# Optimization experiments

Hardware: AMD Instinct MI355X
Metric: run time of the kernel (lower is better)

## Reference

```python
import jax, jax.numpy as jnp
import numpy as np

N, IN, OUT, H = 8192, 128, 64, 4
NEG_SLOPE = 0.2   # GATConv leaky-relu slope
EPS = 1e-5        # BatchNorm1d eps
MASK_VAL = -1e9   # masked_fill value for non-edges (finite for grad safety)


def setup_inputs() -> dict:
    key = jax.random.key(0)
    ks = jax.random.split(key, 5)
    x = jax.random.normal(ks[0], (N, IN), jnp.float32)
    adj = jax.random.randint(ks[1], (N, N), 0, 2, jnp.int32)  # dense 0/1 adjacency
    W = jax.random.normal(ks[2], (H, IN, OUT), jnp.float32) * (1.0 / np.sqrt(IN))
    a_i = jax.random.normal(ks[3], (H, OUT), jnp.float32) * (1.0 / np.sqrt(OUT))
    a_j = jax.random.normal(ks[4], (H, OUT), jnp.float32) * (1.0 / np.sqrt(OUT))
    gamma = jnp.ones((H * OUT,), jnp.float32)   # BN weight
    beta = jnp.zeros((H * OUT,), jnp.float32)   # BN bias
    return {"x": x, "adj": adj, "W": W, "a_i": a_i, "a_j": a_j,
            "gamma": gamma, "beta": beta}


def reference(x, adj, W, a_i, a_j, gamma, beta):
    # --- GATConv (dense adjacency, multi-head, concat) ---
    h = jnp.einsum('ni,hio->hno', x, W)              # [H, N, OUT]
    ei = jnp.einsum('hno,ho->hn', h, a_i)            # [H, N] source scores
    ej = jnp.einsum('hno,ho->hn', h, a_j)            # [H, N] target scores
    coe = ei[:, :, None] + ej[:, None, :]            # [H, N, N]
    coe = jnp.where(coe >= 0, coe, NEG_SLOPE * coe)  # leaky_relu
    coe = jnp.where(adj[None, :, :] == 0, MASK_VAL, coe)
    att = jax.nn.softmax(coe, axis=-1)               # segment softmax over neighbors
    out = jnp.einsum('hnm,hmo->hno', att, h)         # weighted aggregation
    out = jnp.transpose(out, (1, 0, 2)).reshape(N, H * OUT)  # concat heads
    # --- BatchNorm1d (training-mode batch stats over nodes) ---
    mean = jnp.mean(out, axis=0)
    var = jnp.var(out, axis=0)
    out = (out - mean) * jax.lax.rsqrt(var + EPS) * gamma + beta
    # --- ReLU ---
    return jax.nn.relu(out)
```

## Files before the change

### kernel.cpp

```cpp
#include <hip/hip_runtime.h>
#include <hip/hip_bf16.h>

#define NN   8192
#define IND  128
#define OUTD 64
#define NH   4
#define NEG_SLOPE 0.2f
#define BN_EPS 1e-5f

typedef __attribute__((ext_vector_type(8))) short bf16x8;
typedef __attribute__((ext_vector_type(4))) float f32x4;
typedef __attribute__((ext_vector_type(4))) int   i32x4;

static __device__ __forceinline__ short f2bf(float f) {
    union { float f; unsigned u; } v; v.f = f;
    return (short)((v.u + 0x8000u) >> 16);
}

__global__ __launch_bounds__(256) void k0_repackW(const float* __restrict__ W,
                                                  short* __restrict__ WB) {
    int tid = blockIdx.x * 256 + threadIdx.x;
    int o = tid & 63, i = (tid >> 6) & 127, h = tid >> 13;
    WB[((h * 16 + (i >> 3)) * 64 + o) * 8 + (i & 7)] = f2bf(W[(h * 128 + i) * 64 + o]);
}

__global__ __launch_bounds__(256) void k1_feat(const float* __restrict__ x,
                                               const short* __restrict__ WB,
                                               const float* __restrict__ a_i,
                                               const float* __restrict__ a_j,
                                               short* __restrict__ hB,
                                               float* __restrict__ t_Ri,
                                               float* __restrict__ t_E1j, float* __restrict__ t_E2j) {
    int w = threadIdx.x >> 6;
    int l = threadIdx.x & 63;
    int quad = l >> 4, lx = l & 15;
    int rb = blockIdx.x;

    f32x4 acc[4] = {};
#pragma unroll
    for (int ks = 0; ks < 4; ++ks) {
        const float* xp = x + (rb * 16 + lx) * IND + ks * 32 + quad * 8;
        f32x4 xa = *(const f32x4*)xp;
        f32x4 xb = *(const f32x4*)(xp + 4);
        bf16x8 af;
#pragma unroll
        for (int j = 0; j < 4; ++j) { af[j] = f2bf(xa[j]); af[4 + j] = f2bf(xb[j]); }
#pragma unroll
        for (int ot = 0; ot < 4; ++ot) {
            bf16x8 bf = *(const bf16x8*)(WB + ((w * 16 + ks * 4 + quad) * 64 + ot * 16 + lx) * 8);
            acc[ot] = __builtin_amdgcn_mfma_f32_16x16x32_bf16(af, bf, acc[ot], 0, 0, 0);
        }
    }
    float aiv[4], ajv[4];
#pragma unroll
    for (int ot = 0; ot < 4; ++ot) {
        aiv[ot] = a_i[w * 64 + ot * 16 + lx];
        ajv[ot] = a_j[w * 64 + ot * 16 + lx];
    }
#pragma unroll
    for (int reg = 0; reg < 4; ++reg) {
        int row = rb * 16 + quad * 4 + reg;
        float ei = 0.f, ej = 0.f;
#pragma unroll
        for (int ot = 0; ot < 4; ++ot) {
            float hv = acc[ot][reg];
            ei += hv * aiv[ot];
            ej += hv * ajv[ot];
        }
#pragma unroll
        for (int m = 1; m <= 8; m <<= 1) {
            ei += __shfl_xor(ei, m, 64);
            ej += __shfl_xor(ej, m, 64);
        }
        if (lx == reg) {
            t_Ri [w * NN + row] = expf(-0.8f * ei);
            t_E1j[w * NN + row] = expf(ej);
            t_E2j[w * NN + row] = expf(NEG_SLOPE * ej);
        }
#pragma unroll
        for (int ot = 0; ot < 4; ++ot) {
            int o = ot * 16 + lx;
            hB[((w * 1024 + (row >> 3)) * 64 + o) * 8 + (row & 7)] = f2bf(acc[ot][reg]);
        }
    }
}

__global__ __launch_bounds__(256) void k2_attn(const int* __restrict__ adj,
                                               const short* __restrict__ hB,
                                               const float* __restrict__ t_Ri,
                                               const float* __restrict__ t_E1j,
                                               const float* __restrict__ t_E2j,
                                               float* __restrict__ num,
                                               float* __restrict__ Lsum) {
    __shared__ unsigned char smask[64 * 260];
    int tid = threadIdx.x;
    int w = tid >> 6;
    int l = tid & 63;
    int quad = l >> 4, lx = l & 15;
    int rb = blockIdx.x >> 2, ks = blockIdx.x & 3;
    int rowbase = rb * 64;
    int tb = w * NN;
    int k0 = ks * 2048;

    {
        int kc = tid * 8;
#pragma unroll 2
        for (int i = 0; i < 64; ++i) {
            const int* ap = adj + (size_t)(rowbase + i) * NN + k0 + kc;
            i32x4 a0 = *(const i32x4*)ap;
            i32x4 a1 = *(const i32x4*)(ap + 4);
            unsigned m = 0;
#pragma unroll
            for (int j = 0; j < 4; ++j) {
                m |= (a0[j] ? 1u : 0u) << j;
                m |= (a1[j] ? 1u : 0u) << (4 + j);
            }
            smask[i * 260 + tid] = (unsigned char)m;
        }
    }
    __syncthreads();

    float Riv[4];
    int mrow[4];
#pragma unroll
    for (int r = 0; r < 4; ++r) {
        int i = rowbase + r * 16 + lx;
        Riv[r] = t_Ri[tb + i];
        mrow[r] = (r * 16 + lx) * 260 + quad;
    }

    bf16x8 onesf;
#pragma unroll
    for (int j = 0; j < 8; ++j) onesf[j] = (short)0x3F80;

    f32x4 acc[4][4] = {};
    f32x4 accL[4] = {};
    f32x4 pe10, pe11, pe20, pe21;
    bf16x8 pbf[4];
    {
        int kb = k0 + quad * 8;
        pe10 = *(const f32x4*)(t_E1j + tb + kb);
        pe11 = *(const f32x4*)(t_E1j + tb + kb + 4);
        pe20 = *(const f32x4*)(t_E2j + tb + kb);
        pe21 = *(const f32x4*)(t_E2j + tb + kb + 4);
#pragma unroll
        for (int ot = 0; ot < 4; ++ot)
            pbf[ot] = *(const bf16x8*)(hB + ((w * 1024 + (kb >> 3)) * 64 + ot * 16 + lx) * 8);
    }

#pragma unroll 1
    for (int kt = 0; kt < 64; ++kt) {
        f32x4 e1j0 = pe10, e1j1 = pe11;
        f32x4 e2j0 = pe20, e2j1 = pe21;
        bf16x8 bfrag[4];
#pragma unroll
        for (int ot = 0; ot < 4; ++ot) bfrag[ot] = pbf[ot];

        int ktn = (kt + 1) & 63;
        int kbn = k0 + ktn * 32 + quad * 8;
        pe10 = *(const f32x4*)(t_E1j + tb + kbn);
        pe11 = *(const f32x4*)(t_E1j + tb + kbn + 4);
        pe20 = *(const f32x4*)(t_E2j + tb + kbn);
        pe21 = *(const f32x4*)(t_E2j + tb + kbn + 4);
#pragma unroll
        for (int ot = 0; ot < 4; ++ot)
            pbf[ot] = *(const bf16x8*)(hB + ((w * 1024 + (kbn >> 3)) * 64 + ot * 16 + lx) * 8);

        int mc[4];
#pragma unroll
        for (int r = 0; r < 4; ++r) mc[r] = smask[mrow[r] + kt * 4];

        bf16x8 afr[4];
#pragma unroll
        for (int r = 0; r < 4; ++r) {
            union { i32x4 i; bf16x8 b; } af;
#pragma unroll
            for (int jj = 0; jj < 4; ++jj) {
                int j0 = 2 * jj, j1 = 2 * jj + 1;
                float e1A = (j0 < 4) ? e1j0[j0] : e1j1[j0 - 4];
                float e1B = (j1 < 4) ? e1j0[j1] : e1j1[j1 - 4];
                float e2A = (j0 < 4) ? e2j0[j0] : e2j1[j0 - 4];
                float e2B = (j1 < 4) ? e2j0[j1] : e2j1[j1 - 4];
                float p0 = fmaxf(e1A, Riv[r] * e2A);
                float p1 = fmaxf(e1B, Riv[r] * e2B);
                p0 = (mc[r] & (1 << j0)) ? p0 : 0.0f;
                p1 = (mc[r] & (1 << j1)) ? p1 : 0.0f;
                af.i[jj] = (int)__builtin_amdgcn_perm(__float_as_uint(p1),
                                                      __float_as_uint(p0),
                                                      0x07060302);
            }
            afr[r] = af.b;
        }
#pragma unroll
        for (int r = 0; r < 4; ++r)
            accL[r] = __builtin_amdgcn_mfma_f32_16x16x32_bf16(afr[r], onesf, accL[r], 0, 0, 0);
#pragma unroll
        for (int r = 0; r < 4; ++r)
#pragma unroll
            for (int ot = 0; ot < 4; ++ot)
                acc[r][ot] = __builtin_amdgcn_mfma_f32_16x16x32_bf16(afr[r], bfrag[ot], acc[r][ot], 0, 0, 0);
    }

#pragma unroll
    for (int r = 0; r < 4; ++r)
        if (lx == 0)
#pragma unroll
            for (int reg = 0; reg < 4; ++reg)
                atomicAdd(&Lsum[w * NN + rowbase + r * 16 + quad * 4 + reg], accL[r][reg]);
#pragma unroll
    for (int r = 0; r < 4; ++r)
#pragma unroll
        for (int ot = 0; ot < 4; ++ot)
#pragma unroll
            for (int reg = 0; reg < 4; ++reg) {
                int row = rowbase + r * 16 + quad * 4 + reg;
                atomicAdd(&num[row * 256 + w * 64 + ot * 16 + lx], acc[r][ot][reg]);
            }
}

__global__ __launch_bounds__(256) void k3_stats(const float* __restrict__ num,
                                                const float* __restrict__ Lsum,
                                                float* __restrict__ stats) {
    int c = threadIdx.x;
    int h = c >> 6;
    float s = 0.f, s2 = 0.f;
#pragma unroll
    for (int rr = 0; rr < 8; ++rr) {
        int row = blockIdx.x * 8 + rr;
        float val = num[row * 256 + c] / Lsum[h * NN + row];
        s += val; s2 += val * val;
    }
    atomicAdd(&stats[c], s);
    atomicAdd(&stats[c + 256], s2);
}

__global__ __launch_bounds__(256) void k5_apply(const float* __restrict__ num,
                                                const float* __restrict__ Lsum,
                                                const float* __restrict__ stats,
                                                const float* __restrict__ gamma,
                                                const float* __restrict__ beta,
                                                float* __restrict__ out) {
    __shared__ float sbnp[512];
    int c = threadIdx.x;
    float mean = stats[c] * (1.0f / NN);
    float var  = stats[c + 256] * (1.0f / NN) - mean * mean;
    float sc = gamma[c] * rsqrtf(var + BN_EPS);
    sbnp[c] = sc;
    sbnp[c + 256] = beta[c] - mean * sc;
    __syncthreads();

    int g = blockIdx.x * 256 + threadIdx.x;
    f32x4 v = *(const f32x4*)(num + (size_t)g * 4);
    int cb = (g * 4) & 255;
    int row = g >> 6;
    float rL = 1.0f / Lsum[(cb >> 6) * NN + row];
    f32x4 r;
#pragma unroll
    for (int j = 0; j < 4; ++j)
        r[j] = fmaxf((v[j] * rL) * sbnp[cb + j] + sbnp[256 + cb + j], 0.0f);
    *(f32x4*)(out + (size_t)g * 4) = r;
}

extern "C" void kernel_launch(void* const* d_in, const int* in_sizes, int n_in,
                              void* d_out, int out_size, void* d_ws, size_t ws_size,
                              hipStream_t stream) {
    (void)in_sizes; (void)n_in; (void)out_size; (void)ws_size;
    const float* x     = (const float*)d_in[0];
    const int*   adj   = (const int*)d_in[1];
    const float* W     = (const float*)d_in[2];
    const float* a_i   = (const float*)d_in[3];
    const float* a_j   = (const float*)d_in[4];
    const float* gamma = (const float*)d_in[5];
    const float* beta  = (const float*)d_in[6];
    float* out = (float*)d_out;

    char* ws = (char*)d_ws;
    short* WB    = (short*)(ws + 0);
    short* hB    = (short*)(ws + 65536);
    float* t_Ri  = (float*)(ws + 4259840);
    float* t_E1j = t_Ri + 32768;
    float* t_E2j = t_Ri + 2 * 32768;
    float* num   = (float*)(ws + 4784128);
    float* Lsum  = (float*)(ws + 13172736);
    float* stats = (float*)(ws + 13303808);

    hipMemsetAsync(num, 0, 8388608 + 131072 + 2048, stream);

    k0_repackW<<<dim3(128),  dim3(256), 0, stream>>>(W, WB);
    k1_feat   <<<dim3(512),  dim3(256), 0, stream>>>(x, WB, a_i, a_j, hB,
                                                     t_Ri, t_E1j, t_E2j);
    k2_attn   <<<dim3(512),  dim3(256), 0, stream>>>(adj, hB, t_Ri, t_E1j, t_E2j,
                                                     num, Lsum);
    k3_stats  <<<dim3(1024), dim3(256), 0, stream>>>(num, Lsum, stats);
    k5_apply  <<<dim3(2048), dim3(256), 0, stream>>>(num, Lsum, stats, gamma, beta, out);
}
```

Before: 481.6 us.

## Split attention K range into eight chunks and pack mask into per-lane words

The attention kernel now splits the neighbor dimension into eight chunks of 1024 instead of four of 2048, which doubles the grid to 1024 blocks for better occupancy and load balance across CUs. The shared-memory mask is rearranged so each lane reads one 32-bit word holding the mask bytes for its four row groups. That word is prefetched one iteration ahead, replacing four byte loads per step. The cost is twice as many partial-sum atomics or writes into num and Lsum, plus more per-block setup.

```diff
diff --git a/kernel.cpp b/kernel.cpp
--- a/kernel.cpp
+++ b/kernel.cpp
@@ -92,21 +92,25 @@
                                                const float* __restrict__ t_E2j,
                                                float* __restrict__ num,
                                                float* __restrict__ Lsum) {
-    __shared__ unsigned char smask[64 * 260];
+    __shared__ unsigned int swords[128 * 17];
     int tid = threadIdx.x;
     int w = tid >> 6;
     int l = tid & 63;
     int quad = l >> 4, lx = l & 15;
-    int rb = blockIdx.x >> 2, ks = blockIdx.x & 3;
+    int rb = blockIdx.x >> 3, ks = blockIdx.x & 7;
     int rowbase = rb * 64;
     int tb = w * NN;
-    int k0 = ks * 2048;
+    int k0 = ks * 1024;
 
     {
-        int kc = tid * 8;
-#pragma unroll 2
-        for (int i = 0; i < 64; ++i) {
-            const int* ap = adj + (size_t)(rowbase + i) * NN + k0 + kc;
+        unsigned char* sbytes = (unsigned char*)swords;
+        int c = tid & 127;
+        int rhalf = tid >> 7;
+        const int* ap0 = adj + (size_t)(rowbase + rhalf) * NN + k0 + c * 8;
+#pragma unroll 4
+        for (int pass = 0; pass < 32; ++pass) {
+            int row = pass * 2 + rhalf;
+            const int* ap = ap0 + (size_t)(pass * 2) * NN;
             i32x4 a0 = *(const i32x4*)ap;
             i32x4 a1 = *(const i32x4*)(ap + 4);
             unsigned m = 0;
@@ -115,19 +119,15 @@
                 m |= (a0[j] ? 1u : 0u) << j;
                 m |= (a1[j] ? 1u : 0u) << (4 + j);
             }
-            smask[i * 260 + tid] = (unsigned char)m;
+            sbytes[(c * 17 + (row & 15)) * 4 + (row >> 4)] = (unsigned char)m;
         }
     }
     __syncthreads();
 
     float Riv[4];
-    int mrow[4];
-#pragma unroll
-    for (int r = 0; r < 4; ++r) {
-        int i = rowbase + r * 16 + lx;
-        Riv[r] = t_Ri[tb + i];
-        mrow[r] = (r * 16 + lx) * 260 + quad;
-    }
+#pragma unroll
+    for (int r = 0; r < 4; ++r)
+        Riv[r] = t_Ri[tb + rowbase + r * 16 + lx];
 
     bf16x8 onesf;
 #pragma unroll
@@ -137,6 +137,7 @@
     f32x4 accL[4] = {};
     f32x4 pe10, pe11, pe20, pe21;
     bf16x8 pbf[4];
+    unsigned pmw;
     {
         int kb = k0 + quad * 8;
         pe10 = *(const f32x4*)(t_E1j + tb + kb);
@@ -146,17 +147,19 @@
 #pragma unroll
         for (int ot = 0; ot < 4; ++ot)
             pbf[ot] = *(const bf16x8*)(hB + ((w * 1024 + (kb >> 3)) * 64 + ot * 16 + lx) * 8);
+        pmw = swords[quad * 17 + lx];
     }
 
 #pragma unroll 1
-    for (int kt = 0; kt < 64; ++kt) {
+    for (int kt = 0; kt < 32; ++kt) {
         f32x4 e1j0 = pe10, e1j1 = pe11;
         f32x4 e2j0 = pe20, e2j1 = pe21;
+        unsigned mw = pmw;
         bf16x8 bfrag[4];
 #pragma unroll
         for (int ot = 0; ot < 4; ++ot) bfrag[ot] = pbf[ot];
 
-        int ktn = (kt + 1) & 63;
+        int ktn = (kt + 1) & 31;
         int kbn = k0 + ktn * 32 + quad * 8;
         pe10 = *(const f32x4*)(t_E1j + tb + kbn);
         pe11 = *(const f32x4*)(t_E1j + tb + kbn + 4);
@@ -165,14 +168,12 @@
 #pragma unroll
         for (int ot = 0; ot < 4; ++ot)
             pbf[ot] = *(const bf16x8*)(hB + ((w * 1024 + (kbn >> 3)) * 64 + ot * 16 + lx) * 8);
-
-        int mc[4];
-#pragma unroll
-        for (int r = 0; r < 4; ++r) mc[r] = smask[mrow[r] + kt * 4];
+        pmw = swords[(ktn * 4 + quad) * 17 + lx];
 
         bf16x8 afr[4];
 #pragma unroll
         for (int r = 0; r < 4; ++r) {
+            int mc = (mw >> (8 * r)) & 0xff;
             union { i32x4 i; bf16x8 b; } af;
 #pragma unroll
             for (int jj = 0; jj < 4; ++jj) {
@@ -183,8 +184,8 @@
                 float e2B = (j1 < 4) ? e2j0[j1] : e2j1[j1 - 4];
                 float p0 = fmaxf(e1A, Riv[r] * e2A);
                 float p1 = fmaxf(e1B, Riv[r] * e2B);
-                p0 = (mc[r] & (1 << j0)) ? p0 : 0.0f;
-                p1 = (mc[r] & (1 << j1)) ? p1 : 0.0f;
+                p0 = (mc & (1 << j0)) ? p0 : 0.0f;
+                p1 = (mc & (1 << j1)) ? p1 : 0.0f;
                 af.i[jj] = (int)__builtin_amdgcn_perm(__float_as_uint(p1),
                                                       __float_as_uint(p0),
                                                       0x07060302);
@@ -289,7 +290,7 @@
     k0_repackW<<<dim3(128),  dim3(256), 0, stream>>>(W, WB);
     k1_feat   <<<dim3(512),  dim3(256), 0, stream>>>(x, WB, a_i, a_j, hB,
                                                      t_Ri, t_E1j, t_E2j);
-    k2_attn   <<<dim3(512),  dim3(256), 0, stream>>>(adj, hB, t_Ri, t_E1j, t_E2j,
+    k2_attn   <<<dim3(1024), dim3(256), 0, stream>>>(adj, hB, t_Ri, t_E1j, t_E2j,
                                                      num, Lsum);
     k3_stats  <<<dim3(1024), dim3(256), 0, stream>>>(num, Lsum, stats);
     k5_apply  <<<dim3(2048), dim3(256), 0, stream>>>(num, Lsum, stats, gamma, beta, out);
```

New measurement: 492.4 us. 1.02x slower.

## Stage attention B-operand tiles through double-buffered LDS via global_load_lds

Applied to the files above, without the earlier changes.

The attention kernel now copies each head's hB tile into a double-buffered shared-memory buffer with direct global-to-LDS loads, prefetching the next k-tile while the current one is consumed. The E1/E2 and mask values are also double-buffered in registers, the main loop is unrolled by two, and the adjacency staging loop is unrolled further. This aims to hide global load latency behind MFMA work, but it adds a block-wide barrier every iteration and 32KB of LDS per block, which may lower occupancy. The loop may also lack a wait between the async LDS load and the read of that buffer.

```diff
diff --git a/kernel.cpp b/kernel.cpp
--- a/kernel.cpp
+++ b/kernel.cpp
@@ -15,6 +15,16 @@
 static __device__ __forceinline__ short f2bf(float f) {
     union { float f; unsigned u; } v; v.f = f;
     return (short)((v.u + 0x8000u) >> 16);
+}
+
+static __device__ __forceinline__ void stage16(const short* g, short* lbase, int lane) {
+#if defined(__has_builtin) && __has_builtin(__builtin_amdgcn_global_load_lds)
+    __builtin_amdgcn_global_load_lds((const __attribute__((address_space(1))) void*)g,
+                                     (__attribute__((address_space(3))) void*)lbase,
+                                     16, 0, 0);
+#else
+    *(bf16x8*)(lbase + lane * 8) = *(const bf16x8*)g;
+#endif
 }
 
 __global__ __launch_bounds__(256) void k0_repackW(const float* __restrict__ W,
@@ -92,6 +102,7 @@
                                                const float* __restrict__ t_E2j,
                                                float* __restrict__ num,
                                                float* __restrict__ Lsum) {
+    __shared__ short shbuf[2][8192];
     __shared__ unsigned char smask[64 * 260];
     int tid = threadIdx.x;
     int w = tid >> 6;
@@ -102,9 +113,23 @@
     int tb = w * NN;
     int k0 = ks * 2048;
 
+    const short* chunkbase = hB + (size_t)(w * 1024 + (k0 >> 3)) * 512;
+
+    f32x4 te1[2][2], te2[2][2];
+#pragma unroll
+    for (int inst = 0; inst < 4; ++inst)
+        stage16(chunkbase + inst * 512 + l * 8, &shbuf[0][w * 2048 + inst * 512], l);
+    {
+        int kb = k0 + quad * 8;
+        te1[0][0] = *(const f32x4*)(t_E1j + tb + kb);
+        te1[0][1] = *(const f32x4*)(t_E1j + tb + kb + 4);
+        te2[0][0] = *(const f32x4*)(t_E2j + tb + kb);
+        te2[0][1] = *(const f32x4*)(t_E2j + tb + kb + 4);
+    }
+
     {
         int kc = tid * 8;
-#pragma unroll 2
+#pragma unroll 4
         for (int i = 0; i < 64; ++i) {
             const int* ap = adj + (size_t)(rowbase + i) * NN + k0 + kc;
             i32x4 a0 = *(const i32x4*)ap;
@@ -124,10 +149,12 @@
     int mrow[4];
 #pragma unroll
     for (int r = 0; r < 4; ++r) {
-        int i = rowbase + r * 16 + lx;
-        Riv[r] = t_Ri[tb + i];
+        Riv[r] = t_Ri[tb + rowbase + r * 16 + lx];
         mrow[r] = (r * 16 + lx) * 260 + quad;
     }
+    int pm[2][4];
+#pragma unroll
+    for (int r = 0; r < 4; ++r) pm[0][r] = smask[mrow[r]];
 
     bf16x8 onesf;
 #pragma unroll
@@ -135,56 +162,45 @@
 
     f32x4 acc[4][4] = {};
     f32x4 accL[4] = {};
-    f32x4 pe10, pe11, pe20, pe21;
-    bf16x8 pbf[4];
-    {
-        int kb = k0 + quad * 8;
-        pe10 = *(const f32x4*)(t_E1j + tb + kb);
-        pe11 = *(const f32x4*)(t_E1j + tb + kb + 4);
-        pe20 = *(const f32x4*)(t_E2j + tb + kb);
-        pe21 = *(const f32x4*)(t_E2j + tb + kb + 4);
+
+#pragma unroll 2
+    for (int kt = 0; kt < 64; ++kt) {
+        int pp = kt & 1, np = pp ^ 1;
+        int ktn = (kt + 1) & 63;
+
+#pragma unroll
+        for (int inst = 0; inst < 4; ++inst)
+            stage16(chunkbase + ktn * 2048 + inst * 512 + l * 8,
+                    &shbuf[np][w * 2048 + inst * 512], l);
+        int kbn = k0 + ktn * 32 + quad * 8;
+        te1[np][0] = *(const f32x4*)(t_E1j + tb + kbn);
+        te1[np][1] = *(const f32x4*)(t_E1j + tb + kbn + 4);
+        te2[np][0] = *(const f32x4*)(t_E2j + tb + kbn);
+        te2[np][1] = *(const f32x4*)(t_E2j + tb + kbn + 4);
+#pragma unroll
+        for (int r = 0; r < 4; ++r) pm[np][r] = smask[mrow[r] + ktn * 4];
+
+        bf16x8 bfrag[4];
 #pragma unroll
         for (int ot = 0; ot < 4; ++ot)
-            pbf[ot] = *(const bf16x8*)(hB + ((w * 1024 + (kb >> 3)) * 64 + ot * 16 + lx) * 8);
-    }
-
-#pragma unroll 1
-    for (int kt = 0; kt < 64; ++kt) {
-        f32x4 e1j0 = pe10, e1j1 = pe11;
-        f32x4 e2j0 = pe20, e2j1 = pe21;
-        bf16x8 bfrag[4];
-#pragma unroll
-        for (int ot = 0; ot < 4; ++ot) bfrag[ot] = pbf[ot];
-
-        int ktn = (kt + 1) & 63;
-        int kbn = k0 + ktn * 32 + quad * 8;
-        pe10 = *(const f32x4*)(t_E1j + tb + kbn);
-        pe11 = *(const f32x4*)(t_E1j + tb + kbn + 4);
-        pe20 = *(const f32x4*)(t_E2j + tb + kbn);
-        pe21 = *(const f32x4*)(t_E2j + tb + kbn + 4);
-#pragma unroll
-        for (int ot = 0; ot < 4; ++ot)
-            pbf[ot] = *(const bf16x8*)(hB + ((w * 1024 + (kbn >> 3)) * 64 + ot * 16 + lx) * 8);
-
-        int mc[4];
-#pragma unroll
-        for (int r = 0; r < 4; ++r) mc[r] = smask[mrow[r] + kt * 4];
+            bfrag[ot] = *(const bf16x8*)&shbuf[pp][w * 2048 + (quad * 64 + ot * 16 + lx) * 8];
 
         bf16x8 afr[4];
 #pragma unroll
         for (int r = 0; r < 4; ++r) {
+            int mc = pm[pp][r];
             union { i32x4 i; bf16x8 b; } af;
 #pragma unroll
             for (int jj = 0; jj < 4; ++jj) {
                 int j0 = 2 * jj, j1 = 2 * jj + 1;
-                float e1A = (j0 < 4) ? e1j0[j0] : e1j1[j0 - 4];
-                float e1B = (j1 < 4) ? e1j0[j1] : e1j1[j1 - 4];
-                float e2A = (j0 < 4) ? e2j0[j0] : e2j1[j0 - 4];
-                float e2B = (j1 < 4) ? e2j0[j1] : e2j1[j1 - 4];
+                float e1A = (j0 < 4) ? te1[pp][0][j0] : te1[pp][1][j0 - 4];
+                float e1B = (j1 < 4) ? te1[pp][0][j1] : te1[pp][1][j1 - 4];
+                float e2A = (j0 < 4) ? te2[pp][0][j0] : te2[pp][1][j0 - 4];
+                float e2B = (j1 < 4) ? te2[pp][0][j1] : te2[pp][1][j1 - 4];
                 float p0 = fmaxf(e1A, Riv[r] * e2A);
                 float p1 = fmaxf(e1B, Riv[r] * e2B);
-                p0 = (mc[r] & (1 << j0)) ? p0 : 0.0f;
-                p1 = (mc[r] & (1 << j1)) ? p1 : 0.0f;
+                p0 = (mc & (1 << j0)) ? p0 : 0.0f;
+                p1 = (mc & (1 << j1)) ? p1 : 0.0f;
                 af.i[jj] = (int)__builtin_amdgcn_perm(__float_as_uint(p1),
                                                       __float_as_uint(p0),
                                                       0x07060302);
@@ -199,6 +215,8 @@
 #pragma unroll
             for (int ot = 0; ot < 4; ++ot)
                 acc[r][ot] = __builtin_amdgcn_mfma_f32_16x16x32_bf16(afr[r], bfrag[ot], acc[r][ot], 0, 0, 0);
+
+        __syncthreads();
     }
 
 #pragma unroll
```

Result: slower. 548.3 us (+13.9%).
